# Kernel tuning notes

Hardware: AMD Instinct MI355X
Metric: run time of the kernel (lower is better)

## Reference

```python
import jax, jax.numpy as jnp
import numpy as np

N = 4096
F_IN = 3000
F_OUT = 64
NEG_INF = jnp.float32(-9e15)


def _xavier(key, shape):
    fan_in, fan_out = shape[0], shape[-1]
    limit = (6.0 / (fan_in + fan_out)) ** 0.5
    return jax.random.uniform(key, shape, jnp.float32, -limit, limit)


def setup_inputs() -> dict:
    key = jax.random.key(0)
    ks = jax.random.split(key, 20)
    feat = jax.random.normal(ks[0], (N, F_IN), jnp.float32)
    feat_a = jax.random.normal(ks[1], (N, F_IN), jnp.float32)
    eye = jnp.eye(N, dtype=jnp.float32)
    adj = jnp.maximum((jax.random.uniform(ks[2], (N, N)) < 0.008).astype(jnp.float32), eye)
    graph_neigh = jnp.maximum((jax.random.uniform(ks[3], (N, N)) < 0.008).astype(jnp.float32), eye)
    return {
        "feat": feat,
        "feat_a": feat_a,
        "adj": adj,
        "graph_neigh": graph_neigh,
        "weight1": _xavier(ks[4], (F_IN, F_OUT)),
        "weight2": _xavier(ks[5], (F_OUT, F_IN)),
        "att_W": _xavier(ks[6], (F_OUT, F_OUT)),
        "a_src": _xavier(ks[7], (F_OUT, 1)),
        "a_dst": _xavier(ks[8], (F_OUT, 1)),
        "mlp_W1": _xavier(ks[9], (F_OUT, 256)),
        "mlp_b1": jnp.zeros((256,), jnp.float32),
        "mlp_W2": _xavier(ks[10], (256, 128)),
        "mlp_b2": jnp.zeros((128,), jnp.float32),
        "mlp_W3": _xavier(ks[11], (128, F_OUT)),
        "mlp_b3": jnp.zeros((F_OUT,), jnp.float32),
        "dmlp_W1": _xavier(ks[12], (F_OUT, 128)),
        "dmlp_b1": jnp.zeros((128,), jnp.float32),
        "dmlp_W2": _xavier(ks[13], (128, F_OUT)),
        "dmlp_b2": jnp.zeros((F_OUT,), jnp.float32),
        "bil_W": _xavier(ks[14], (F_OUT, F_OUT)),
        "bil_b": jnp.zeros((1,), jnp.float32),
    }


def reference(feat, feat_a, adj, graph_neigh,
              weight1, weight2, att_W, a_src, a_dst,
              mlp_W1, mlp_b1, mlp_W2, mlp_b2, mlp_W3, mlp_b3,
              dmlp_W1, dmlp_b1, dmlp_W2, dmlp_b2, bil_W, bil_b):
    relu = jax.nn.relu

    def attention(h):
        Wh = h @ att_W                      # [N, F_OUT]
        e = Wh @ a_src + (Wh @ a_dst).T     # [N, N]
        e = jnp.where(e > 0, e, 0.2 * e)    # LeakyReLU(0.2)
        e = jnp.where(adj > 0, e, NEG_INF)  # mask non-edges
        return jax.nn.softmax(e, axis=1) @ Wh

    def mlp(x):
        x = relu(x @ mlp_W1 + mlp_b1)
        x = relu(x @ mlp_W2 + mlp_b2)
        return x @ mlp_W3 + mlp_b3

    def dmlp(x):  # discriminator MLP: n_h -> 128 -> n_h
        return relu(x @ dmlp_W1 + dmlp_b1) @ dmlp_W2 + dmlp_b2

    def readout(emb):  # AvgReadout + L2 normalize
        g = (graph_neigh @ emb) / jnp.sum(graph_neigh, axis=1, keepdims=True)
        return g / jnp.maximum(jnp.linalg.norm(g, axis=1, keepdims=True), 1e-12)

    def bilinear(x, y):  # nn.Bilinear(n_h, n_h, 1)
        return (jnp.einsum('ni,ij,nj->n', x, bil_W, y) + bil_b)[:, None]

    def disc(c, h_pl, h_mi):
        c, h_pl, h_mi = dmlp(c), dmlp(h_pl), dmlp(h_mi)
        return jnp.concatenate([bilinear(h_pl, c), bilinear(h_mi, c)], axis=1)

    z = mlp(attention(feat @ weight1))
    hiden_emb = z
    h = adj @ (z @ weight2)                 # spmm(adj, z @ weight2)
    emb = relu(z)
    z_a = mlp(attention(feat_a @ weight1))
    emb_a = relu(z_a)
    g = jax.nn.sigmoid(readout(emb))
    g_a = jax.nn.sigmoid(readout(emb_a))
    ret = disc(g, emb, emb_a)
    ret_a = disc(g_a, emb_a, emb)
    return (hiden_emb, h, ret, ret_a)
```

## Files before the change

### kernel.cpp

```cpp
#include <hip/hip_runtime.h>

#define NN   4096
#define FIN  3000
#define MAXN 128

typedef unsigned short u16;
typedef __bf16 bf16x8 __attribute__((ext_vector_type(8)));
typedef float f32x16 __attribute__((ext_vector_type(16)));

__device__ __forceinline__ float bf2f(u16 u) { union { unsigned int i; float f; } v; v.i = ((unsigned int)u) << 16; return v.f; }
__device__ __forceinline__ u16 f2bf(float f) {
    union { float f; unsigned int i; } v; v.f = f;
    return (u16)((v.i + 0x7FFFu + ((v.i >> 16) & 1u)) >> 16);
}
__device__ __forceinline__ bf16x8 bzero8() {
    union { unsigned long long q[2]; bf16x8 v; } u; u.q[0] = 0ull; u.q[1] = 0ull; return u.v;
}
__device__ __forceinline__ f32x16 fzero16() {
    f32x16 v;
    #pragma unroll
    for (int i = 0; i < 16; i++) v[i] = 0.f;
    return v;
}
__device__ __forceinline__ void gload_lds16(const float* src, void* ldsbase) {
    __builtin_amdgcn_global_load_lds(
        (const __attribute__((address_space(1))) void*)src,
        (__attribute__((address_space(3))) void*)ldsbase, 16, 0, 0);
}

__global__ __launch_bounds__(1024) void k_detect(const u16* __restrict__ feat, int* __restrict__ flag)
{
    __shared__ int tot;
    if (threadIdx.x == 0) tot = 0;
    __syncthreads();
    int ins = 0;
    for (int i = threadIdx.x; i < 16384; i += 1024) {
        u16 u = feat[i];
        int e = (u >> 7) & 0xFF;
        if (u != 0 && (e < 90 || e > 160)) ins++;
    }
    atomicAdd(&tot, ins);
    __syncthreads();
    if (threadIdx.x == 0) *flag = (tot > 1024) ? 1 : 0;
}

__global__ __launch_bounds__(256) void k_convw(const int* __restrict__ flag,
    const void* s0, const void* s1, const void* s2, const void* s3,
    const void* s4, const void* s5, const void* s6, const void* s7,
    const void* s8, const void* s9, const void* s10, const void* s11,
    const void* s12, const void* s13, const void* s14, const void* s15,
    float* __restrict__ dst)
{
    const void* srcs[16] = {s0,s1,s2,s3,s4,s5,s6,s7,s8,s9,s10,s11,s12,s13,s14,s15};
    const int offs[16] = {0,192000,196096,196160,196224,212608,212864,245632,245760,253952,254016,262208,262336,270528,270592,274688};
    const int ns[16]   = {192000,4096,64,64,16384,256,32768,128,8192,64,8192,128,8192,64,4096,1};
    int seg = blockIdx.y;
    int i = blockIdx.x * 256 + threadIdx.x;
    if (i >= ns[seg]) return;
    float v = (*flag) ? ((const float*)srcs[seg])[i] : bf2f(((const u16*)srcs[seg])[i]);
    dst[offs[seg] + i] = v;
}

__global__ __launch_bounds__(256) void k_convw2t(const int* __restrict__ flag,
    const void* __restrict__ src, u16* __restrict__ WH, u16* __restrict__ WL)
{
    int i = blockIdx.x * 256 + threadIdx.x;
    if (i >= 3008 * 64) return;
    int n = i >> 6, k = i & 63;
    float v = 0.f;
    if (n < FIN)
        v = (*flag) ? ((const float*)src)[(size_t)k * FIN + n]
                    : bf2f(((const u16*)src)[(size_t)k * FIN + n]);
    u16 h = f2bf(v);
    float r = v - bf2f(h);
    WH[i] = h;
    WL[i] = f2bf(r);
}

__global__ __launch_bounds__(256) void k_convw1t(const int* __restrict__ flag,
    const void* __restrict__ w1src, u16* __restrict__ BtH, u16* __restrict__ BtL)
{
    int i = blockIdx.x * 256 + threadIdx.x;
    if (i >= 64 * 3008) return;
    int c = i / 3008, k = i - c * 3008;
    float v = 0.f;
    if (k < 3000)
        v = (*flag) ? ((const float*)w1src)[(size_t)k * 64 + c]
                    : bf2f(((const u16*)w1src)[(size_t)k * 64 + c]);
    u16 h = f2bf(v);
    float r = v - bf2f(h);
    BtH[(size_t)c * 3008 + k] = h;
    BtL[(size_t)c * 3008 + k] = f2bf(r);
}

__global__ __launch_bounds__(256) void k_build_csr(const int* __restrict__ flag,
    const void* __restrict__ Av, const void* __restrict__ Gv,
    int* __restrict__ aCnt, int* __restrict__ aIdx,
    int* __restrict__ gCnt, int* __restrict__ gIdx)
{
    bool isf = (*flag != 0);
    const void* M = blockIdx.y ? Gv : Av;
    int* cnt = blockIdx.y ? gCnt : aCnt;
    int* idx = blockIdx.y ? gIdx : aIdx;
    int row = blockIdx.x, t = threadIdx.x;
    int c0 = t * 16;
    unsigned int mask = 0; int my = 0;
    if (isf) {
        const float4* r = (const float4*)((const float*)M + (size_t)row * NN + c0);
        union { float4 q[4]; float f[16]; } u;
        u.q[0] = r[0]; u.q[1] = r[1]; u.q[2] = r[2]; u.q[3] = r[3];
        #pragma unroll
        for (int j = 0; j < 16; j++) if (u.f[j] != 0.f) { mask |= 1u << j; my++; }
    } else {
        const uint4* r = (const uint4*)((const u16*)M + (size_t)row * NN + c0);
        union { uint4 q[2]; u16 h[16]; } u;
        u.q[0] = r[0]; u.q[1] = r[1];
        #pragma unroll
        for (int j = 0; j < 16; j++) if (u.h[j] != 0) { mask |= 1u << j; my++; }
    }
    __shared__ int sc[256];
    sc[t] = my;
    __syncthreads();
    for (int d = 1; d < 256; d <<= 1) {
        int v = (t >= d) ? sc[t - d] : 0;
        __syncthreads();
        sc[t] += v;
        __syncthreads();
    }
    int pos = sc[t] - my;
    for (int j = 0; j < 16; j++) {
        if (mask & (1u << j)) {
            if (pos < MAXN) idx[(size_t)row * MAXN + pos] = c0 + j;
            pos++;
        }
    }
    if (t == 0) { int total = sc[255]; cnt[row] = (total < MAXN) ? total : MAXN; }
}

__global__ __launch_bounds__(512) void k_featgemm_mfma(const int* __restrict__ flag,
    const void* __restrict__ F0v, const void* __restrict__ F1v,
    const u16* __restrict__ BtH, float* __restrict__ X0, float* __restrict__ X1)
{
    if (*flag) return;
    const u16* F = (const u16*)(blockIdx.y ? F1v : F0v);
    float* X = blockIdx.y ? X1 : X0;
    int r0 = blockIdx.x * 32;
    int tid = threadIdx.x;
    int w  = tid >> 6;
    int l  = tid & 63;
    int lr = l & 31;
    int kg = l >> 5;
    const u16* arow = F   + (size_t)(r0 + lr) * FIN + kg * 8;
    const u16* b0p  = BtH + (size_t)lr * 3008 + kg * 8;
    const u16* b1p  = BtH + (size_t)(lr + 32) * 3008 + kg * 8;
    f32x16 acc0 = fzero16(), acc1 = fzero16();
    #pragma unroll 4
    for (int s = w; s < 188; s += 8) {
        int kk = s * 16;
        bf16x8 a;
        if (kk + kg * 8 < FIN) a = *(const bf16x8*)(arow + kk);
        else                   a = bzero8();
        bf16x8 b0 = *(const bf16x8*)(b0p + kk);
        bf16x8 b1 = *(const bf16x8*)(b1p + kk);
        acc0 = __builtin_amdgcn_mfma_f32_32x32x16_bf16(a, b0, acc0, 0, 0, 0);
        acc1 = __builtin_amdgcn_mfma_f32_32x32x16_bf16(a, b1, acc1, 0, 0, 0);
    }
    __shared__ float red[8][2048];
    float* rp = red[w];
    #pragma unroll
    for (int reg = 0; reg < 16; reg++) {
        int row = (reg & 3) + 8 * (reg >> 2) + 4 * kg;
        rp[row * 64 + lr] = acc0[reg];
    }
    #pragma unroll
    for (int reg = 0; reg < 16; reg++) {
        int row = (reg & 3) + 8 * (reg >> 2) + 4 * kg;
        rp[row * 64 + 32 + lr] = acc1[reg];
    }
    __syncthreads();
    for (int i = tid; i < 2048; i += 512) {
        float s0 = 0.f;
        #pragma unroll
        for (int j = 0; j < 8; j++) s0 += red[j][i];
        X[(size_t)r0 * 64 + i] = s0;
    }
}

__global__ __launch_bounds__(256) void k_featgemm_mfma_f32(const int* __restrict__ flag,
    const void* __restrict__ F0v, const void* __restrict__ F1v,
    const u16* __restrict__ BtH, const u16* __restrict__ BtL,
    float* __restrict__ X0, float* __restrict__ X1)
{
    if (!*flag) return;
    const float* F = (const float*)(blockIdx.y ? F1v : F0v);
    float* X = blockIdx.y ? X1 : X0;
    int tid = threadIdx.x;
    int w  = tid >> 6;
    int l  = tid & 63;
    int lr = l & 31;
    int kg = l >> 5;
    int wr = w >> 1, wc = w & 1;
    int r0 = blockIdx.x * 64;
    int chunk = blockIdx.z;
    int sbeg = chunk * 12;
    int nsteps = (chunk == 3) ? 11 : 12;

    __shared__ char lds[3][16384];

    const float* Fb = F + (size_t)r0 * FIN;
    int arow = 32 * wr + lr;
    int acol = 32 * wc + lr;
    const u16* bh = BtH + (size_t)acol * 3008;
    const u16* bl = BtL + (size_t)acol * 3008;
    int slin = (w * 16) * 256 + l * 16;
    f32x16 acc = fzero16();

    auto STAGE = [&](int s, int buf) {
        int kbase = (sbeg + s) * 64;
        #pragma unroll
        for (int j = 0; j < 4; j++) {
            int lin = slin + j * 1024;
            int row = lin >> 8;
            int off = (lin & 255) ^ ((row & 15) << 4);
            gload_lds16(Fb + (size_t)row * FIN + kbase + (off >> 2),
                        &lds[buf][(w * 16 + j * 4) * 256]);
        }
    };

    STAGE(0, 0);
    STAGE(1, 1);

    for (int s = 0; s < nsteps; ++s) {
        if (s < nsteps - 1) asm volatile("s_waitcnt vmcnt(4)" ::: "memory");
        else                asm volatile("s_waitcnt vmcnt(0)" ::: "memory");
        __builtin_amdgcn_s_barrier();
        if (s + 2 < nsteps) STAGE(s + 2, (s + 2) % 3);
        const char* lb = lds[s % 3];
        int kk0 = (sbeg + s) * 64;
        #pragma unroll
        for (int s16 = 0; s16 < 4; s16++) {
            int offu = s16 * 64 + kg * 32;
            int o0 = offu        ^ ((arow & 15) << 4);
            int o1 = (offu + 16) ^ ((arow & 15) << 4);
            float4 a0 = *(const float4*)(lb + arow * 256 + o0);
            float4 a1 = *(const float4*)(lb + arow * 256 + o1);
            float av[8] = {a0.x, a0.y, a0.z, a0.w, a1.x, a1.y, a1.z, a1.w};
            bf16x8 ah, al;
            #pragma unroll
            for (int jj = 0; jj < 8; jj++) {
                __bf16 hv = (__bf16)av[jj];
                ah[jj] = hv;
                al[jj] = (__bf16)(av[jj] - (float)hv);
            }
            int kk = kk0 + s16 * 16 + kg * 8;
            bf16x8 H = *(const bf16x8*)(bh + kk);
            bf16x8 L = *(const bf16x8*)(bl + kk);
            acc = __builtin_amdgcn_mfma_f32_32x32x16_bf16(ah, H, acc, 0, 0, 0);
            acc = __builtin_amdgcn_mfma_f32_32x32x16_bf16(al, H, acc, 0, 0, 0);
            acc = __builtin_amdgcn_mfma_f32_32x32x16_bf16(ah, L, acc, 0, 0, 0);
        }
    }

    #pragma unroll
    for (int reg = 0; reg < 16; reg++) {
        int row = (reg & 3) + 8 * (reg >> 2) + 4 * kg;
        atomicAdd(&X[(size_t)(r0 + 32 * wr + row) * 64 + acol], acc[reg]);
    }
}

__global__ __launch_bounds__(256) void k_whsd(
    const float* __restrict__ X1, const float* __restrict__ X2,
    const float* __restrict__ AW, const float* __restrict__ asrc, const float* __restrict__ adst,
    float* __restrict__ Wh1, float* __restrict__ Wh2,
    float* __restrict__ s1, float* __restrict__ s2,
    float* __restrict__ d1, float* __restrict__ d2)
{
    const float* X = blockIdx.y ? X2 : X1;
    float* Wh = blockIdx.y ? Wh2 : Wh1;
    float* sv = blockIdx.y ? s2 : s1;
    float* dv = blockIdx.y ? d2 : d1;
    __shared__ float aw[64][65];
    __shared__ float x[4][65];
    int tid = threadIdx.x;
    for (int i = tid; i < 4096; i += 256) aw[i >> 6][i & 63] = AW[i];
    int g = tid >> 6, c = tid & 63;
    int row = blockIdx.x * 4 + g;
    x[g][c] = X[(size_t)row * 64 + c];
    __syncthreads();
    float acc = 0.f;
    #pragma unroll 16
    for (int k = 0; k < 64; k++) acc += x[g][k] * aw[k][c];
    Wh[(size_t)row * 64 + c] = acc;
    float vs = acc * asrc[c];
    float vd = acc * adst[c];
    #pragma unroll
    for (int off = 32; off > 0; off >>= 1) { vs += __shfl_down(vs, off); vd += __shfl_down(vd, off); }
    if (c == 0) { sv[row] = vs; dv[row] = vd; }
}

__global__ __launch_bounds__(128) void k_attn(
    const int* __restrict__ cnt, const int* __restrict__ idx,
    const float* __restrict__ s1, const float* __restrict__ s2,
    const float* __restrict__ d1, const float* __restrict__ d2,
    const float* __restrict__ Wh1, const float* __restrict__ Wh2,
    float* __restrict__ A1, float* __restrict__ A2)
{
    const float* sp = blockIdx.y ? s2 : s1;
    const float* dp = blockIdx.y ? d2 : d1;
    const float* Wh = blockIdx.y ? Wh2 : Wh1;
    float* A = blockIdx.y ? A2 : A1;
    int row = blockIdx.x, tid = threadIdx.x;
    int n = cnt[row];
    __shared__ int js[MAXN];
    __shared__ float ps[MAXN];
    __shared__ float red2[2];
    __shared__ float ared[2][64];
    for (int k = tid; k < n; k += 128) js[k] = idx[(size_t)row * MAXN + k];
    __syncthreads();
    float si = sp[row];
    float m = -3.0e38f;
    for (int k = tid; k < n; k += 128) {
        float e = si + dp[js[k]];
        e = e > 0.f ? e : 0.2f * e;
        ps[k] = e;
        m = fmaxf(m, e);
    }
    #pragma unroll
    for (int off = 32; off > 0; off >>= 1) m = fmaxf(m, __shfl_down(m, off));
    if ((tid & 63) == 0) red2[tid >> 6] = m;
    __syncthreads();
    m = fmaxf(red2[0], red2[1]);
    __syncthreads();
    float zz = 0.f;
    for (int k = tid; k < n; k += 128) {
        float p = __expf(ps[k] - m);
        ps[k] = p;
        zz += p;
    }
    #pragma unroll
    for (int off = 32; off > 0; off >>= 1) zz += __shfl_down(zz, off);
    if ((tid & 63) == 0) red2[tid >> 6] = zz;
    __syncthreads();
    float Z = red2[0] + red2[1];
    Z = fmaxf(Z, 1e-20f);
    int f = tid & 63, half = tid >> 6;
    float acc = 0.f;
    for (int k = half; k < n; k += 2) acc += ps[k] * Wh[(size_t)js[k] * 64 + f];
    ared[half][f] = acc;
    __syncthreads();
    if (tid < 64) A[(size_t)row * 64 + f] = (ared[0][f] + ared[1][f]) / Z;
}

__global__ __launch_bounds__(256) void k_mlp(const int* __restrict__ flag,
    const float* __restrict__ A1, const float* __restrict__ A2,
    const float* __restrict__ W1, const float* __restrict__ b1,
    const float* __restrict__ W2, const float* __restrict__ b2,
    const float* __restrict__ W3, const float* __restrict__ b3,
    float* __restrict__ Z1, float* __restrict__ Z2, void* __restrict__ hidenv)
{
    const float* A = blockIdx.y ? A2 : A1;
    float* Z = blockIdx.y ? Z2 : Z1;
    int row0 = blockIdx.x * 4, tid = threadIdx.x;
    __shared__ float x[4][64], h1[4][256], h2[4][128];
    {
        int r = tid >> 6, c = tid & 63;
        x[r][c] = A[(size_t)(row0 + r) * 64 + c];
    }
    __syncthreads();
    {
        float a0 = b1[tid], a1v = a0, a2v = a0, a3v = a0;
        #pragma unroll 8
        for (int k = 0; k < 64; k++) {
            float w = W1[k * 256 + tid];
            a0 += x[0][k] * w; a1v += x[1][k] * w; a2v += x[2][k] * w; a3v += x[3][k] * w;
        }
        h1[0][tid] = fmaxf(a0, 0.f);  h1[1][tid] = fmaxf(a1v, 0.f);
        h1[2][tid] = fmaxf(a2v, 0.f); h1[3][tid] = fmaxf(a3v, 0.f);
    }
    __syncthreads();
    if (tid < 128) {
        float a0 = b2[tid], a1v = a0, a2v = a0, a3v = a0;
        #pragma unroll 8
        for (int k = 0; k < 256; k++) {
            float w = W2[k * 128 + tid];
            a0 += h1[0][k] * w; a1v += h1[1][k] * w; a2v += h1[2][k] * w; a3v += h1[3][k] * w;
        }
        h2[0][tid] = fmaxf(a0, 0.f);  h2[1][tid] = fmaxf(a1v, 0.f);
        h2[2][tid] = fmaxf(a2v, 0.f); h2[3][tid] = fmaxf(a3v, 0.f);
    }
    __syncthreads();
    if (tid < 64) {
        float a[4];
        a[0] = a[1] = a[2] = a[3] = b3[tid];
        #pragma unroll 8
        for (int k = 0; k < 128; k++) {
            float w = W3[k * 64 + tid];
            a[0] += h2[0][k] * w; a[1] += h2[1][k] * w; a[2] += h2[2][k] * w; a[3] += h2[3][k] * w;
        }
        bool isf = (*flag != 0);
        #pragma unroll
        for (int r = 0; r < 4; r++) {
            size_t ei = (size_t)(row0 + r) * 64 + tid;
            Z[ei] = a[r];
            if (blockIdx.y == 0) {
                if (isf) ((float*)hidenv)[ei] = a[r];
                else     ((u16*)hidenv)[ei] = f2bf(a[r]);
            }
        }
    }
}

__global__ __launch_bounds__(64) void k_spmm(
    const int* __restrict__ cnt, const int* __restrict__ idx,
    const float* __restrict__ Z, float* __restrict__ T)
{
    int row = blockIdx.x, f = threadIdx.x;
    int n = cnt[row];
    const int* ir = idx + (size_t)row * MAXN;
    float acc = 0.f;
    for (int k = 0; k < n; k++) acc += Z[(size_t)ir[k] * 64 + f];
    T[(size_t)row * 64 + f] = acc;
}

__global__ __launch_bounds__(256) void k_hgemm_mfma(const int* __restrict__ flag,
    const float* __restrict__ T, const u16* __restrict__ WH, const u16* __restrict__ WL,
    void* __restrict__ outv)
{
    bool isf = (*flag != 0);
    int tid = threadIdx.x;
    int w = tid >> 6, l = tid & 63, lr = l & 31, kg = l >> 5;
    int ct = blockIdx.y * 4 + w;
    if (ct >= 94) return;
    int r0 = blockIdx.x * 32, c0 = ct * 32;
    const float* tp = T + (size_t)(r0 + lr) * 64 + kg * 8;
    bf16x8 ah[4], al[4];
    #pragma unroll
    for (int s = 0; s < 4; s++) {
        float4 p0 = *(const float4*)(tp + s * 16);
        float4 p1 = *(const float4*)(tp + s * 16 + 4);
        float av[8] = {p0.x, p0.y, p0.z, p0.w, p1.x, p1.y, p1.z, p1.w};
        #pragma unroll
        for (int j = 0; j < 8; j++) {
            __bf16 hv = (__bf16)av[j];
            ah[s][j] = hv;
            al[s][j] = (__bf16)(av[j] - (float)hv);
        }
    }
    const u16* bh = WH + (size_t)(c0 + lr) * 64 + kg * 8;
    const u16* bl = WL + (size_t)(c0 + lr) * 64 + kg * 8;
    f32x16 acc = fzero16();
    #pragma unroll
    for (int s = 0; s < 4; s++) {
        bf16x8 vh = *(const bf16x8*)(bh + s * 16);
        bf16x8 vl = *(const bf16x8*)(bl + s * 16);
        acc = __builtin_amdgcn_mfma_f32_32x32x16_bf16(ah[s], vh, acc, 0, 0, 0);
        acc = __builtin_amdgcn_mfma_f32_32x32x16_bf16(al[s], vh, acc, 0, 0, 0);
        acc = __builtin_amdgcn_mfma_f32_32x32x16_bf16(ah[s], vl, acc, 0, 0, 0);
    }
    int col = c0 + lr;
    bool cok = col < FIN;
    #pragma unroll
    for (int reg = 0; reg < 16; reg++) {
        int row = (reg & 3) + 8 * (reg >> 2) + 4 * kg;
        size_t ei = 262144 + (size_t)(r0 + row) * FIN + col;
        if (cok) {
            if (isf) ((float*)outv)[ei] = acc[reg];
            else     ((u16*)outv)[ei] = f2bf(acc[reg]);
        }
    }
}

__global__ __launch_bounds__(64) void k_readout(
    const int* __restrict__ cnt, const int* __restrict__ idx,
    const float* __restrict__ Z1, const float* __restrict__ Z2,
    float* __restrict__ G1, float* __restrict__ G2)
{
    const float* Z = blockIdx.y ? Z2 : Z1;
    float* G = blockIdx.y ? G2 : G1;
    int row = blockIdx.x, f = threadIdx.x;
    int n = cnt[row];
    const int* ir = idx + (size_t)row * MAXN;
    float acc = 0.f;
    for (int k = 0; k < n; k++) acc += fmaxf(Z[(size_t)ir[k] * 64 + f], 0.f);
    acc /= (float)(n > 0 ? n : 1);
    float sq = acc * acc;
    #pragma unroll
    for (int off = 32; off > 0; off >>= 1) sq += __shfl_down(sq, off);
    sq = __shfl(sq, 0);
    float nrm = fmaxf(sqrtf(sq), 1e-12f);
    float v = acc / nrm;
    G[(size_t)row * 64 + f] = 1.f / (1.f + __expf(-v));
}

__global__ __launch_bounds__(128) void k_dmlp(
    const float* __restrict__ z, const float* __restrict__ za,
    const float* __restrict__ g, const float* __restrict__ ga,
    const float* __restrict__ W1, const float* __restrict__ b1,
    const float* __restrict__ W2, const float* __restrict__ b2,
    float* __restrict__ De, float* __restrict__ Dea,
    float* __restrict__ Dg, float* __restrict__ Dga)
{
    int w = blockIdx.y;
    const float* X = (w == 0) ? z : (w == 1) ? za : (w == 2) ? g : ga;
    float* O = (w == 0) ? De : (w == 1) ? Dea : (w == 2) ? Dg : Dga;
    int doRelu = (w < 2);
    int row0 = blockIdx.x * 4, tid = threadIdx.x;
    __shared__ float x[4][64], h1[4][128];
    for (int i = tid; i < 256; i += 128) {
        int r = i >> 6, c = i & 63;
        float v = X[(size_t)(row0 + r) * 64 + c];
        x[r][c] = doRelu ? fmaxf(v, 0.f) : v;
    }
    __syncthreads();
    {
        float a0 = b1[tid], a1v = a0, a2v = a0, a3v = a0;
        #pragma unroll 8
        for (int k = 0; k < 64; k++) {
            float w_ = W1[k * 128 + tid];
            a0 += x[0][k] * w_; a1v += x[1][k] * w_; a2v += x[2][k] * w_; a3v += x[3][k] * w_;
        }
        h1[0][tid] = fmaxf(a0, 0.f);  h1[1][tid] = fmaxf(a1v, 0.f);
        h1[2][tid] = fmaxf(a2v, 0.f); h1[3][tid] = fmaxf(a3v, 0.f);
    }
    __syncthreads();
    if (tid < 64) {
        float a[4];
        a[0] = a[1] = a[2] = a[3] = b2[tid];
        #pragma unroll 8
        for (int k = 0; k < 128; k++) {
            float w_ = W2[k * 64 + tid];
            a[0] += h1[0][k] * w_; a[1] += h1[1][k] * w_; a[2] += h1[2][k] * w_; a[3] += h1[3][k] * w_;
        }
        #pragma unroll
        for (int r = 0; r < 4; r++) O[(size_t)(row0 + r) * 64 + tid] = a[r];
    }
}

__global__ __launch_bounds__(256) void k_bilin_pre(
    const float* __restrict__ Dg, const float* __restrict__ Dga,
    const float* __restrict__ BW, float* __restrict__ V1, float* __restrict__ V2)
{
    const float* Y = blockIdx.y ? Dga : Dg;
    float* V = blockIdx.y ? V2 : V1;
    __shared__ float bw[64][65];
    __shared__ float y[4][65];
    int tid = threadIdx.x;
    for (int i = tid; i < 4096; i += 256) bw[i >> 6][i & 63] = BW[i];
    int g = tid >> 6, k = tid & 63;
    int rbase = blockIdx.x * 64;
    for (int it = 0; it < 16; it++) {
        __syncthreads();
        int r = rbase + it * 4 + g;
        y[g][k] = Y[(size_t)r * 64 + k];
        __syncthreads();
        float acc = 0.f;
        #pragma unroll 16
        for (int j = 0; j < 64; j++) acc += y[g][j] * bw[k][j];
        V[(size_t)r * 64 + k] = acc;
    }
}

__global__ __launch_bounds__(256) void k_bilin_dot(const int* __restrict__ flag,
    const float* __restrict__ De, const float* __restrict__ Dea,
    const float* __restrict__ V1, const float* __restrict__ V2,
    const float* __restrict__ bb, void* __restrict__ outv)
{
    int w = blockIdx.y;
    const float* X = (w == 0 || w == 3) ? De : Dea;
    const float* V = (w <= 1) ? V1 : V2;
    size_t bse = (w <= 1) ? (size_t)12550144 : (size_t)12558336;
    int col = (w == 0 || w == 2) ? 0 : 1;
    int g = threadIdx.x >> 6, k = threadIdx.x & 63;
    int row = blockIdx.x * 4 + g;
    float v = X[(size_t)row * 64 + k] * V[(size_t)row * 64 + k];
    #pragma unroll
    for (int off = 32; off > 0; off >>= 1) v += __shfl_down(v, off);
    if (k == 0) {
        float r = v + bb[0];
        size_t ei = bse + (size_t)row * 2 + col;
        if (*flag) ((float*)outv)[ei] = r;
        else       ((u16*)outv)[ei] = f2bf(r);
    }
}

extern "C" void kernel_launch(void* const* d_in, const int* in_sizes, int n_in,
                              void* d_out, int out_size, void* d_ws, size_t ws_size,
                              hipStream_t stream) {
    const void* feat   = d_in[0];
    const void* feat_a = d_in[1];
    const void* adj    = d_in[2];
    const void* gn     = d_in[3];
    const void* w1     = d_in[4];
    const void* w2     = d_in[5];
    const void* attW   = d_in[6];
    const void* a_src  = d_in[7];
    const void* a_dst  = d_in[8];
    const void* mW1    = d_in[9];
    const void* mb1    = d_in[10];
    const void* mW2    = d_in[11];
    const void* mb2    = d_in[12];
    const void* mW3    = d_in[13];
    const void* mb3    = d_in[14];
    const void* dW1    = d_in[15];
    const void* db1    = d_in[16];
    const void* dW2    = d_in[17];
    const void* db2    = d_in[18];
    const void* bW     = d_in[19];
    const void* bb     = d_in[20];
    (void)in_sizes; (void)n_in; (void)out_size;

    char* wsb = (char*)d_ws;
    int*   flag = (int*)wsb;
    float* T    = (float*)(wsb + 256);
    u16*   W2tH = (u16*)(wsb + 256 + 1048576);
    u16*   W2tL = W2tH + 3008 * 64;
    (void)ws_size;

    char* sc = (char*)d_out + 1048576;
    size_t soff = 0;
    auto salloc = [&](size_t nbytes) -> void* {
        void* p = (void*)(sc + soff);
        soff += (nbytes + 255) & ~(size_t)255;
        return p;
    };
    const size_t NV = (size_t)NN * 64;
    float* wA   = (float*)salloc((size_t)274689 * 4);
    int*   aCnt = (int*)salloc(NN * 4);
    int*   gCnt = (int*)salloc(NN * 4);
    int*   aIdx = (int*)salloc((size_t)NN * MAXN * 4);
    int*   gIdx = (int*)salloc((size_t)NN * MAXN * 4);
    float* X1  = (float*)salloc(NV * 4);
    float* X2  = (float*)salloc(NV * 4);
    float* Wh1 = (float*)salloc(NV * 4);
    float* Wh2 = (float*)salloc(NV * 4);
    float* A1  = (float*)salloc(NV * 4);
    float* A2  = (float*)salloc(NV * 4);
    float* z   = (float*)salloc(NV * 4);
    float* za  = (float*)salloc(NV * 4);
    float* g   = (float*)salloc(NV * 4);
    float* ga  = (float*)salloc(NV * 4);
    float* De  = (float*)salloc(NV * 4);
    float* Dea = (float*)salloc(NV * 4);
    float* Dg  = (float*)salloc(NV * 4);
    float* Dga = (float*)salloc(NV * 4);
    float* s1  = (float*)salloc(NN * 4);
    float* s2  = (float*)salloc(NN * 4);
    float* d1  = (float*)salloc(NN * 4);
    float* d2  = (float*)salloc(NN * 4);

    float* w1f   = wA + 0;
    float* attWf = wA + 192000;
    float* asrcf = wA + 196096;
    float* adstf = wA + 196160;
    float* mW1f  = wA + 196224;
    float* mb1f  = wA + 212608;
    float* mW2f  = wA + 212864;
    float* mb2f  = wA + 245632;
    float* mW3f  = wA + 245760;
    float* mb3f  = wA + 253952;
    float* dW1f  = wA + 254016;
    float* db1f  = wA + 262208;
    float* dW2f  = wA + 262336;
    float* db2f  = wA + 270528;
    float* bWf   = wA + 270592;
    float* bbf   = wA + 274688;

    u16* BtH = (u16*)De;
    u16* BtL = (u16*)Dea;

    k_detect<<<1, 1024, 0, stream>>>((const u16*)feat, flag);
    k_convw<<<dim3(750, 16), 256, 0, stream>>>(flag,
        w1, attW, a_src, a_dst, mW1, mb1, mW2, mb2, mW3, mb3,
        dW1, db1, dW2, db2, bW, bb, wA);
    k_convw2t<<<752, 256, 0, stream>>>(flag, w2, W2tH, W2tL);
    k_convw1t<<<752, 256, 0, stream>>>(flag, w1, BtH, BtL);
    k_build_csr<<<dim3(NN, 2), 256, 0, stream>>>(flag, adj, gn, aCnt, aIdx, gCnt, gIdx);
    hipMemsetAsync(X1, 0, 2 * NV * 4, stream);
    k_featgemm_mfma<<<dim3(NN / 32, 2), 512, 0, stream>>>(flag, feat, feat_a, BtH, X1, X2);
    k_featgemm_mfma_f32<<<dim3(NN / 64, 2, 4), 256, 0, stream>>>(flag, feat, feat_a, BtH, BtL, X1, X2);
    k_whsd<<<dim3(NN / 4, 2), 256, 0, stream>>>(X1, X2, attWf, asrcf, adstf, Wh1, Wh2, s1, s2, d1, d2);
    k_attn<<<dim3(NN, 2), 128, 0, stream>>>(aCnt, aIdx, s1, s2, d1, d2, Wh1, Wh2, A1, A2);
    k_mlp<<<dim3(NN / 4, 2), 256, 0, stream>>>(flag, A1, A2, mW1f, mb1f, mW2f, mb2f, mW3f, mb3f, z, za, d_out);
    k_readout<<<dim3(NN, 2), 64, 0, stream>>>(gCnt, gIdx, z, za, g, ga);
    k_dmlp<<<dim3(NN / 4, 4), 128, 0, stream>>>(z, za, g, ga, dW1f, db1f, dW2f, db2f, De, Dea, Dg, Dga);
    k_bilin_pre<<<dim3(64, 2), 256, 0, stream>>>(Dg, Dga, bWf, A1, A2);
    k_bilin_dot<<<dim3(NN / 4, 4), 256, 0, stream>>>(flag, De, Dea, A1, A2, bbf, d_out);
    k_spmm<<<NN, 64, 0, stream>>>(aCnt, aIdx, z, T);
    k_hgemm_mfma<<<dim3(NN / 32, 24), 256, 0, stream>>>(flag, T, W2tH, W2tL, d_out);
}
```

Measured before the change: 448.9 us.

## Stage split-bf16 weight tiles through LDS with double-buffered async loads

The feature-projection GEMM kernel now loads the hi/lo bf16 weight fragments into LDS with global_load_lds alongside the feature tile, instead of each lane reading them directly from global memory inside the MFMA loop. The pipeline moves from a 3-stage buffer with 16KB slots to a 2-stage double buffer with 32KB slots. The next stage is issued before waiting, and a second barrier at the end of each step protects buffer reuse. This targets the latency of scattered global weight reads, at the cost of an extra barrier per step and reduced prefetch depth.

```diff
diff --git a/kernel.cpp b/kernel.cpp
--- a/kernel.cpp
+++ b/kernel.cpp
@@ -22,7 +22,7 @@
     for (int i = 0; i < 16; i++) v[i] = 0.f;
     return v;
 }
-__device__ __forceinline__ void gload_lds16(const float* src, void* ldsbase) {
+__device__ __forceinline__ void gload_lds16(const void* src, void* ldsbase) {
     __builtin_amdgcn_global_load_lds(
         (const __attribute__((address_space(1))) void*)src,
         (__attribute__((address_space(3))) void*)ldsbase, 16, 0, 0);
@@ -205,38 +205,52 @@
     int sbeg = chunk * 12;
     int nsteps = (chunk == 3) ? 11 : 12;
 
-    __shared__ char lds[3][16384];
+    __shared__ char lds[2][32768];
 
     const float* Fb = F + (size_t)r0 * FIN;
     int arow = 32 * wr + lr;
     int acol = 32 * wc + lr;
-    const u16* bh = BtH + (size_t)acol * 3008;
-    const u16* bl = BtL + (size_t)acol * 3008;
     int slin = (w * 16) * 256 + l * 16;
     f32x16 acc = fzero16();
 
     auto STAGE = [&](int s, int buf) {
         int kbase = (sbeg + s) * 64;
+        char* base = lds[buf];
         #pragma unroll
         for (int j = 0; j < 4; j++) {
             int lin = slin + j * 1024;
             int row = lin >> 8;
             int off = (lin & 255) ^ ((row & 15) << 4);
-            gload_lds16(Fb + (size_t)row * FIN + kbase + (off >> 2),
-                        &lds[buf][(w * 16 + j * 4) * 256]);
+            gload_lds16((const void*)(Fb + (size_t)row * FIN + kbase + (off >> 2)),
+                        base + (w * 16 + j * 4) * 256);
+        }
+        #pragma unroll
+        for (int j = 0; j < 2; j++) {
+            int kgrp = w * 2 + j;
+            gload_lds16((const void*)(BtH + (size_t)l * 3008 + kbase + kgrp * 8),
+                        base + 16384 + kgrp * 1024);
+        }
+        #pragma unroll
+        for (int j = 0; j < 2; j++) {
+            int kgrp = w * 2 + j;
+            gload_lds16((const void*)(BtL + (size_t)l * 3008 + kbase + kgrp * 8),
+                        base + 24576 + kgrp * 1024);
         }
     };
 
     STAGE(0, 0);
-    STAGE(1, 1);
 
     for (int s = 0; s < nsteps; ++s) {
-        if (s < nsteps - 1) asm volatile("s_waitcnt vmcnt(4)" ::: "memory");
-        else                asm volatile("s_waitcnt vmcnt(0)" ::: "memory");
+        if (s + 1 < nsteps) {
+            STAGE(s + 1, (s + 1) & 1);
+            asm volatile("s_waitcnt vmcnt(8)" ::: "memory");
+        } else {
+            asm volatile("s_waitcnt vmcnt(0)" ::: "memory");
+        }
         __builtin_amdgcn_s_barrier();
-        if (s + 2 < nsteps) STAGE(s + 2, (s + 2) % 3);
-        const char* lb = lds[s % 3];
-        int kk0 = (sbeg + s) * 64;
+        const char* lb = lds[s & 1];
+        const char* Bh = lb + 16384;
+        const char* Bl = lb + 24576;
         #pragma unroll
         for (int s16 = 0; s16 < 4; s16++) {
             int offu = s16 * 64 + kg * 32;
@@ -252,13 +266,14 @@
                 ah[jj] = hv;
                 al[jj] = (__bf16)(av[jj] - (float)hv);
             }
-            int kk = kk0 + s16 * 16 + kg * 8;
-            bf16x8 H = *(const bf16x8*)(bh + kk);
-            bf16x8 L = *(const bf16x8*)(bl + kk);
+            int kgrp = s16 * 2 + kg;
+            bf16x8 H = *(const bf16x8*)(Bh + (kgrp * 64 + acol) * 16);
+            bf16x8 L = *(const bf16x8*)(Bl + (kgrp * 64 + acol) * 16);
             acc = __builtin_amdgcn_mfma_f32_32x32x16_bf16(ah, H, acc, 0, 0, 0);
             acc = __builtin_amdgcn_mfma_f32_32x32x16_bf16(al, H, acc, 0, 0, 0);
             acc = __builtin_amdgcn_mfma_f32_32x32x16_bf16(ah, L, acc, 0, 0, 0);
         }
+        __builtin_amdgcn_s_barrier();
     }
 
     #pragma unroll
```

Result: no change. 446.2 us (-0.6%).
